# Kernel tuning notes

Measured on AMD Instinct MI355X. Metric: run time of the kernel, lower is better.

Reference implementation:

```python
import jax, jax.numpy as jnp
import numpy as np
from jax import lax

DIM = 1024
DIM_INNER = 2048  # int(dim * expansion_factor)


def log_g(x):
    # log-space g(x): where(x>=0, log(relu(x)+0.5), -softplus(-x))
    return jnp.where(x >= 0, jnp.log(jax.nn.relu(x) + 0.5), -jax.nn.softplus(-x))


def heinsen_associative_scan_log(log_coeffs, log_values):
    # parallel log-space linear recurrence over the sequence axis (axis=1)
    a_star = jnp.cumsum(log_coeffs, axis=1)
    log_h0_plus_b_star = lax.cumlogsumexp(log_values - a_star, axis=1)
    return a_star + log_h0_plus_b_star


def setup_inputs() -> dict:
    key = jax.random.key(0)
    k_x, k_w1, k_w2 = jax.random.split(key, 3)
    x = jax.random.normal(k_x, (4, 4096, DIM), dtype=jnp.float32)
    # Linear(dim, 2*dim_inner, bias=False): store as [in, out] for x @ W
    W_hg = jax.random.normal(k_w1, (DIM, 2 * DIM_INNER), dtype=jnp.float32) * (1.0 / np.sqrt(DIM))
    W_out = jax.random.normal(k_w2, (DIM_INNER, DIM), dtype=jnp.float32) * (1.0 / np.sqrt(DIM_INNER))
    return {"x": x, "W_hg": W_hg, "W_out": W_out}


def reference(x, W_hg, W_out):
    # x: [b, s, dim]
    hg = jnp.einsum('bsd,de->bse', x, W_hg)  # [b, s, 2*dim_inner]
    hidden, gate = jnp.split(hg, 2, axis=-1)
    log_coeffs = -jax.nn.softplus(gate)        # log(1 - z)
    log_z = -jax.nn.softplus(-gate)            # log z
    log_values = log_z + log_g(hidden)
    log_h = heinsen_associative_scan_log(log_coeffs, log_values)  # [b, s, dim_inner]
    out = jnp.exp(log_h)
    return jnp.einsum('bse,ed->bsd', out, W_out)
```

## Files before the change

### kernel.cpp

```cpp
#include <hip/hip_runtime.h>
#include <cmath>

#define DIM 1024
#define DIM_INNER 2048
#define BATCH 4
#define SEQ 4096
#define MTOT (BATCH * SEQ)
#define CHUNK 32
#define NCHUNK (SEQ / CHUNK)

typedef __bf16 bf16x8 __attribute__((ext_vector_type(8)));
typedef short short8_t __attribute__((ext_vector_type(8)));
typedef float floatx4 __attribute__((ext_vector_type(4)));
typedef unsigned short u16x4 __attribute__((ext_vector_type(4)));
typedef unsigned int uint4_t __attribute__((ext_vector_type(4)));
typedef float float4_t __attribute__((ext_vector_type(4)));
typedef unsigned short ushort_t;

template <int N> struct IC { static constexpr int v = N; };
template <bool B> struct BC { static constexpr bool v = B; };

#define LGKM_SB(n) do { asm volatile("s_waitcnt lgkmcnt(" #n ")" ::: "memory"); \
                        __builtin_amdgcn_sched_barrier(0); } while (0)
#define SCHED0() __builtin_amdgcn_sched_barrier(0)
#define SBAR() __builtin_amdgcn_s_barrier()

__device__ __forceinline__ unsigned short f2bf(float f) {
  unsigned int u = __builtin_bit_cast(unsigned int, f);
  u += 0x7fffu + ((u >> 16) & 1u);
  return (unsigned short)(u >> 16);
}
__device__ __forceinline__ float bflo2f(unsigned int u) {
  return __builtin_bit_cast(float, u << 16);
}
__device__ __forceinline__ float bfhi2f(unsigned int u) {
  return __builtin_bit_cast(float, u & 0xffff0000u);
}

__device__ __forceinline__ void lclv_fast(float h, float g, float& lc, float& lv) {
  float eg = __expf(-fabsf(g));
  float sp = fmaxf(g, 0.f) + __logf(1.f + eg);
  lc = -sp;
  float eh = __expf(h);
  float t  = (h >= 0.f) ? (h + 0.5f) : (1.f + eh);
  float lt = __logf(t);
  float lg = (h >= 0.f) ? lt : (h - lt);
  lv = g + lc + lg;
}
__device__ __forceinline__ float logaddexp_f(float a, float b) {
  float m = fmaxf(a, b);
  return m + __logf(1.f + __expf(-fabsf(a - b)));
}

__device__ __forceinline__ void async_copy16(const ushort_t* g, ushort_t* l) {
  __builtin_amdgcn_global_load_lds(
      (const __attribute__((address_space(1))) void*)g,
      (__attribute__((address_space(3))) void*)l, 16, 0, 0);
}

__global__ __launch_bounds__(256) void convert_f32_bf16(
    const float* __restrict__ src, ushort_t* __restrict__ dst) {
  int i = blockIdx.x * 256 + threadIdx.x;
  float4 v = ((const float4*)src)[i];
  u16x4 o = {f2bf(v.x), f2bf(v.y), f2bf(v.z), f2bf(v.w)};
  ((u16x4*)dst)[i] = o;
}

__global__ __launch_bounds__(256) void transpose_f32_bf16(
    const float* __restrict__ src, ushort_t* __restrict__ dst, int K, int N) {
  __shared__ float tile[32][33];
  int tx = threadIdx.x & 31, ty = threadIdx.x >> 5;
  int n0 = blockIdx.x * 32, k0 = blockIdx.y * 32;
#pragma unroll
  for (int i = 0; i < 4; i++) {
    int k = ty + i * 8;
    tile[k][tx] = src[(size_t)(k0 + k) * N + n0 + tx];
  }
  __syncthreads();
#pragma unroll
  for (int i = 0; i < 4; i++) {
    int r = ty + i * 8;
    dst[(size_t)(n0 + r) * K + k0 + tx] = f2bf(tile[tx][r]);
  }
}

#define G1_NT (DIM / 64)
#define G2_NT (DIM_INNER / 64)

__global__ __launch_bounds__(512, 2) void gemm1_fused(
    const ushort_t* __restrict__ Xbf, const ushort_t* __restrict__ Wt,
    unsigned int* __restrict__ LCLV,
    float* __restrict__ Asum, float* __restrict__ Lend, int nbch) {
  __shared__ __align__(16) ushort_t lds[81920];

  const int tid = threadIdx.x;
  const int wv = tid >> 6;
  const int lane = tid & 63;
  const int wr = wv >> 2;
  const int wc = wv & 3;
  const int l15 = lane & 15;
  const int quad = lane >> 4;

  const int nwg = gridDim.x * gridDim.y;
  const int lin = blockIdx.y * gridDim.x + blockIdx.x;
  const int qchunk = nwg >> 3;
  const int wid = (lin & 7) * qchunk + (lin >> 3);
  const int n0 = (wid & 15) * 128;
  const int m0 = (wid >> 4) * 256;

  int aSrc[2][2], bSrc[2][2];
  int dstE[2];
#pragma unroll
  for (int L = 0; L < 2; L++) {
    int e = L * 512 + tid;
    int row = e >> 3, slot = e & 7;
    int sw = (slot ^ (row & 7)) << 3;
    dstE[L] = e * 8;
#pragma unroll
    for (int half = 0; half < 2; half++) {
      aSrc[half][L] = (m0 + half * 128 + row) * DIM + sw;
      int br = half * 128 + row;
      int grow = n0 + ((br >> 6) << 5) + (br & 31) + ((br & 32) ? DIM_INNER : 0);
      bSrc[half][L] = grow * DIM + sw;
    }
  }

  auto stageA = [&](int kt, int half, int buf) {
#pragma unroll
    for (int L = 0; L < 2; L++)
      async_copy16(Xbf + aSrc[half][L] + kt * 64,
                   lds + buf * 16384 + half * 8192 + dstE[L]);
  };
  auto stageB = [&](int kt, int half, int buf) {
#pragma unroll
    for (int L = 0; L < 2; L++)
      async_copy16(Wt + bSrc[half][L] + kt * 64,
                   lds + 49152 + buf * 16384 + half * 8192 + dstE[L]);
  };

  const int swz0 = ((quad ^ (l15 & 7)) << 3);
  const int swz1 = (((4 | quad) ^ (l15 & 7)) << 3);
  const int aB0 = wr * 8192 + l15 * 64 + swz0;
  const int aB1 = wr * 8192 + l15 * 64 + swz1;
  const int bB0 = wc * 4096 + l15 * 64 + swz0;
  const int bB1 = wc * 4096 + l15 * 64 + swz1;

  auto readA = [&](int buf, int mf, int ks) -> bf16x8 {
    const ushort_t* p = lds + buf * 16384 + (ks ? aB1 : aB0) + mf * 1024;
    return __builtin_bit_cast(bf16x8, *(const short8_t*)p);
  };
  auto readB = [&](int buf, int nf, int ks) -> bf16x8 {
    const ushort_t* p = lds + 49152 + buf * 16384 + (ks ? bB1 : bB0) + nf * 1024;
    return __builtin_bit_cast(bf16x8, *(const short8_t*)p);
  };

  floatx4 acc[8][4];
#pragma unroll
  for (int i = 0; i < 8; i++)
#pragma unroll
    for (int j = 0; j < 4; j++) acc[i][j] = (floatx4){0.f, 0.f, 0.f, 0.f};

  bf16x8 aF[4][2], b0F[2][2], b1F[2][2];

  auto mma4 = [&](auto MA, auto MC, auto J, bf16x8 (&bX)[2][2]) {
#pragma unroll
    for (int jj = 0; jj < 2; jj++)
#pragma unroll
      for (int ks = 0; ks < 2; ks++)
        acc[MC.v][J.v + jj] = __builtin_amdgcn_mfma_f32_16x16x32_bf16(
            aF[MA.v][ks], bX[jj][ks], acc[MC.v][J.v + jj], 0, 0, 0);
  };
  auto mmaRow = [&](auto J, bf16x8 (&bvec)[2]) {
#pragma unroll
    for (int m = 0; m < 4; m++)
#pragma unroll
      for (int ks = 0; ks < 2; ks++)
        acc[m][J.v] = __builtin_amdgcn_mfma_f32_16x16x32_bf16(
            aF[m][ks], bvec[ks], acc[m][J.v], 0, 0, 0);
  };

  int bufA = 0, bufB = 0, bufAn = 2, bufBn = 1;

  auto tileBody = [&](int kb, int ka, auto STB, auto STA, auto VMALL) {
    aF[0][0] = readA(bufA, 0, 0); aF[0][1] = readA(bufA, 0, 1);
    b0F[0][0] = readB(bufB, 0, 0); b0F[0][1] = readB(bufB, 0, 1);
    b0F[1][0] = readB(bufB, 1, 0); b0F[1][1] = readB(bufB, 1, 1);
    SCHED0();
    aF[1][0] = readA(bufA, 1, 0); aF[1][1] = readA(bufA, 1, 1);
    SCHED0();
    aF[2][0] = readA(bufA, 2, 0); aF[2][1] = readA(bufA, 2, 1);
    SCHED0();
    aF[3][0] = readA(bufA, 3, 0); aF[3][1] = readA(bufA, 3, 1);
    SCHED0();
    if constexpr (STB.v) stageB(kb, 0, bufBn);
    SBAR();
    __builtin_amdgcn_s_setprio(1);
    LGKM_SB(6); mma4(IC<0>{}, IC<0>{}, IC<0>{}, b0F);
    LGKM_SB(4); mma4(IC<1>{}, IC<1>{}, IC<0>{}, b0F);
    LGKM_SB(2); mma4(IC<2>{}, IC<2>{}, IC<0>{}, b0F);
    LGKM_SB(0); mma4(IC<3>{}, IC<3>{}, IC<0>{}, b0F);
    __builtin_amdgcn_s_setprio(0);
    SBAR();

    b1F[0][0] = readB(bufB, 2, 0); b1F[0][1] = readB(bufB, 2, 1);
    SCHED0();
    b1F[1][0] = readB(bufB, 3, 0); b1F[1][1] = readB(bufB, 3, 1);
    SCHED0();
    if constexpr (STB.v) stageB(kb, 1, bufBn);
    SBAR();
    __builtin_amdgcn_s_setprio(1);
    LGKM_SB(2); mmaRow(IC<2>{}, b1F[0]);
    LGKM_SB(0); mmaRow(IC<3>{}, b1F[1]);
    __builtin_amdgcn_s_setprio(0);
    SBAR();

    aF[0][0] = readA(bufA, 4, 0); aF[0][1] = readA(bufA, 4, 1);
    SCHED0();
    aF[1][0] = readA(bufA, 5, 0); aF[1][1] = readA(bufA, 5, 1);
    SCHED0();
    aF[2][0] = readA(bufA, 6, 0); aF[2][1] = readA(bufA, 6, 1);
    SCHED0();
    aF[3][0] = readA(bufA, 7, 0); aF[3][1] = readA(bufA, 7, 1);
    SCHED0();
    if constexpr (STA.v) stageA(ka, 0, bufAn);
    SBAR();
    __builtin_amdgcn_s_setprio(1);
    LGKM_SB(6); mma4(IC<0>{}, IC<4>{}, IC<2>{}, b1F);
    LGKM_SB(4); mma4(IC<1>{}, IC<5>{}, IC<2>{}, b1F);
    LGKM_SB(2); mma4(IC<2>{}, IC<6>{}, IC<2>{}, b1F);
    LGKM_SB(0); mma4(IC<3>{}, IC<7>{}, IC<2>{}, b1F);
    __builtin_amdgcn_s_setprio(0);
    SBAR();

    if constexpr (STA.v) stageA(ka, 1, bufAn);
    SCHED0();
    if constexpr (STA.v) {
      asm volatile("s_waitcnt vmcnt(4)" ::: "memory");
    } else if constexpr (VMALL.v) {
      asm volatile("s_waitcnt vmcnt(0)" ::: "memory");
    }
    SBAR();
    __builtin_amdgcn_s_setprio(1);
    mma4(IC<0>{}, IC<4>{}, IC<0>{}, b0F);
    mma4(IC<1>{}, IC<5>{}, IC<0>{}, b0F);
    mma4(IC<2>{}, IC<6>{}, IC<0>{}, b0F);
    mma4(IC<3>{}, IC<7>{}, IC<0>{}, b0F);
    __builtin_amdgcn_s_setprio(0);
    SBAR();
  };

  stageB(0, 0, 0); stageB(0, 1, 0);
  stageA(0, 0, 0); stageA(0, 1, 0);
  stageA(1, 0, 1); stageA(1, 1, 1);
  asm volatile("s_waitcnt vmcnt(4)" ::: "memory");
  SBAR();

  for (int u = 0; u < G1_NT - 2; u++) {
    tileBody(u + 1, u + 2, BC<true>{}, BC<true>{}, BC<false>{});
    bufA = (bufA == 2) ? 0 : bufA + 1;
    bufAn = (bufAn == 2) ? 0 : bufAn + 1;
    bufB ^= 1; bufBn ^= 1;
  }
  tileBody(G1_NT - 1, 0, BC<true>{}, BC<false>{}, BC<true>{});
  bufA = (bufA == 2) ? 0 : bufA + 1;
  bufB ^= 1;
  tileBody(0, 0, BC<false>{}, BC<false>{}, BC<false>{});

#pragma unroll
  for (int c2 = 0; c2 < 4; c2++) {
    float hA[2][2], hL[2][2];
#pragma unroll
    for (int mh = 0; mh < 2; mh++) {
      int mf = c2 * 2 + mh;
#pragma unroll
      for (int j = 0; j < 2; j++) {
        int col = n0 + wc * 32 + j * 16 + l15;
        float sA = 0.f, sL = -INFINITY;
#pragma unroll
        for (int r = 0; r < 4; r++) {
          int row = m0 + wr * 128 + mf * 16 + quad * 4 + r;
          float lc, lv;
          lclv_fast(acc[mf][j][r], acc[mf][j + 2][r], lc, lv);
          unsigned int pk = ((unsigned int)f2bf(lv) << 16) | (unsigned int)f2bf(lc);
          LCLV[(size_t)row * DIM_INNER + col] = pk;
          float lcr = bflo2f(pk), lvr = bfhi2f(pk);
          sL = logaddexp_f(sL + lcr, lvr);
          sA += lcr;
        }
        float A = sA, L = sL;
#pragma unroll
        for (int st = 16; st <= 32; st <<= 1) {
          float Ao = __shfl_xor(A, st, 64);
          float Lo = __shfl_xor(L, st, 64);
          bool upper = (lane & st) != 0;
          L = upper ? logaddexp_f(Lo + A, L) : logaddexp_f(L + Ao, Lo);
          A = A + Ao;
        }
        hA[mh][j] = A;
        hL[mh][j] = L;
      }
    }
#pragma unroll
    for (int j = 0; j < 2; j++) {
      float A = hA[0][j] + hA[1][j];
      float L = logaddexp_f(hL[0][j] + hA[1][j], hL[1][j]);
      if (quad == 0) {
        int cg = (m0 + wr * 128 + c2 * 32) >> 5;
        int bz = cg >> 7;
        int cs = cg & (NCHUNK - 1);
        int col = n0 + wc * 32 + j * 16 + l15;
        size_t sidx = (size_t)cs * nbch + (size_t)bz * DIM_INNER + col;
        Asum[sidx] = A;
        Lend[sidx] = L;
      }
    }
  }
}

__global__ __launch_bounds__(512, 2) void gemm2(
    const ushort_t* __restrict__ Hbf, const ushort_t* __restrict__ Wot,
    float* __restrict__ OUT) {
  __shared__ __align__(16) ushort_t lds[81920];

  const int tid = threadIdx.x;
  const int wv = tid >> 6;
  const int lane = tid & 63;
  const int wr = wv >> 2;
  const int wc = wv & 3;
  const int l15 = lane & 15;
  const int quad = lane >> 4;
  const int n0 = blockIdx.x * 256;
  const int m0 = blockIdx.y * 256;

  int aSrc[2][2], bSrc[2][2];
  int dstE[2];
#pragma unroll
  for (int L = 0; L < 2; L++) {
    int e = L * 512 + tid;
    int row = e >> 3, slot = e & 7;
    int sw = (slot ^ (row & 7)) << 3;
    dstE[L] = e * 8;
#pragma unroll
    for (int half = 0; half < 2; half++) {
      aSrc[half][L] = (m0 + half * 128 + row) * DIM_INNER + sw;
      bSrc[half][L] = (n0 + half * 128 + row) * DIM_INNER + sw;
    }
  }

  auto stageA = [&](int kt, int half, int buf) {
#pragma unroll
    for (int L = 0; L < 2; L++)
      async_copy16(Hbf + aSrc[half][L] + kt * 64,
                   lds + buf * 16384 + half * 8192 + dstE[L]);
  };
  auto stageB = [&](int kt, int half, int buf) {
#pragma unroll
    for (int L = 0; L < 2; L++)
      async_copy16(Wot + bSrc[half][L] + kt * 64,
                   lds + 49152 + buf * 16384 + half * 8192 + dstE[L]);
  };

  const int swz0 = ((quad ^ (l15 & 7)) << 3);
  const int swz1 = (((4 | quad) ^ (l15 & 7)) << 3);
  const int aB0 = wr * 8192 + l15 * 64 + swz0;
  const int aB1 = wr * 8192 + l15 * 64 + swz1;
  const int bB0 = wc * 4096 + l15 * 64 + swz0;
  const int bB1 = wc * 4096 + l15 * 64 + swz1;

  auto readA = [&](int buf, int mf, int ks) -> bf16x8 {
    const ushort_t* p = lds + buf * 16384 + (ks ? aB1 : aB0) + mf * 1024;
    return __builtin_bit_cast(bf16x8, *(const short8_t*)p);
  };
  auto readB = [&](int buf, int nf, int ks) -> bf16x8 {
    const ushort_t* p = lds + 49152 + buf * 16384 + (ks ? bB1 : bB0) + nf * 1024;
    return __builtin_bit_cast(bf16x8, *(const short8_t*)p);
  };

  floatx4 acc[8][4];
#pragma unroll
  for (int i = 0; i < 8; i++)
#pragma unroll
    for (int j = 0; j < 4; j++) acc[i][j] = (floatx4){0.f, 0.f, 0.f, 0.f};

  bf16x8 aF[4][2], b0F[2][2], b1F[2][2];

  auto mma4 = [&](auto MA, auto MC, auto J, bf16x8 (&bX)[2][2]) {
#pragma unroll
    for (int jj = 0; jj < 2; jj++)
#pragma unroll
      for (int ks = 0; ks < 2; ks++)
        acc[MC.v][J.v + jj] = __builtin_amdgcn_mfma_f32_16x16x32_bf16(
            aF[MA.v][ks], bX[jj][ks], acc[MC.v][J.v + jj], 0, 0, 0);
  };
  auto mmaRow = [&](auto J, bf16x8 (&bvec)[2]) {
#pragma unroll
    for (int m = 0; m < 4; m++)
#pragma unroll
      for (int ks = 0; ks < 2; ks++)
        acc[m][J.v] = __builtin_amdgcn_mfma_f32_16x16x32_bf16(
            aF[m][ks], bvec[ks], acc[m][J.v], 0, 0, 0);
  };

  int bufA = 0, bufB = 0, bufAn = 2, bufBn = 1;

  auto tileBody = [&](int kb, int ka, auto STB, auto STA, auto VMALL) {
    aF[0][0] = readA(bufA, 0, 0); aF[0][1] = readA(bufA, 0, 1);
    b0F[0][0] = readB(bufB, 0, 0); b0F[0][1] = readB(bufB, 0, 1);
    b0F[1][0] = readB(bufB, 1, 0); b0F[1][1] = readB(bufB, 1, 1);
    SCHED0();
    aF[1][0] = readA(bufA, 1, 0); aF[1][1] = readA(bufA, 1, 1);
    SCHED0();
    aF[2][0] = readA(bufA, 2, 0); aF[2][1] = readA(bufA, 2, 1);
    SCHED0();
    aF[3][0] = readA(bufA, 3, 0); aF[3][1] = readA(bufA, 3, 1);
    SCHED0();
    if constexpr (STB.v) stageB(kb, 0, bufBn);
    SBAR();
    __builtin_amdgcn_s_setprio(1);
    LGKM_SB(6); mma4(IC<0>{}, IC<0>{}, IC<0>{}, b0F);
    LGKM_SB(4); mma4(IC<1>{}, IC<1>{}, IC<0>{}, b0F);
    LGKM_SB(2); mma4(IC<2>{}, IC<2>{}, IC<0>{}, b0F);
    LGKM_SB(0); mma4(IC<3>{}, IC<3>{}, IC<0>{}, b0F);
    __builtin_amdgcn_s_setprio(0);
    SBAR();

    b1F[0][0] = readB(bufB, 2, 0); b1F[0][1] = readB(bufB, 2, 1);
    SCHED0();
    b1F[1][0] = readB(bufB, 3, 0); b1F[1][1] = readB(bufB, 3, 1);
    SCHED0();
    if constexpr (STB.v) stageB(kb, 1, bufBn);
    SBAR();
    __builtin_amdgcn_s_setprio(1);
    LGKM_SB(2); mmaRow(IC<2>{}, b1F[0]);
    LGKM_SB(0); mmaRow(IC<3>{}, b1F[1]);
    __builtin_amdgcn_s_setprio(0);
    SBAR();

    aF[0][0] = readA(bufA, 4, 0); aF[0][1] = readA(bufA, 4, 1);
    SCHED0();
    aF[1][0] = readA(bufA, 5, 0); aF[1][1] = readA(bufA, 5, 1);
    SCHED0();
    aF[2][0] = readA(bufA, 6, 0); aF[2][1] = readA(bufA, 6, 1);
    SCHED0();
    aF[3][0] = readA(bufA, 7, 0); aF[3][1] = readA(bufA, 7, 1);
    SCHED0();
    if constexpr (STA.v) stageA(ka, 0, bufAn);
    SBAR();
    __builtin_amdgcn_s_setprio(1);
    LGKM_SB(6); mma4(IC<0>{}, IC<4>{}, IC<2>{}, b1F);
    LGKM_SB(4); mma4(IC<1>{}, IC<5>{}, IC<2>{}, b1F);
    LGKM_SB(2); mma4(IC<2>{}, IC<6>{}, IC<2>{}, b1F);
    LGKM_SB(0); mma4(IC<3>{}, IC<7>{}, IC<2>{}, b1F);
    __builtin_amdgcn_s_setprio(0);
    SBAR();

    if constexpr (STA.v) stageA(ka, 1, bufAn);
    SCHED0();
    if constexpr (STA.v) {
      asm volatile("s_waitcnt vmcnt(4)" ::: "memory");
    } else if constexpr (VMALL.v) {
      asm volatile("s_waitcnt vmcnt(0)" ::: "memory");
    }
    SBAR();
    __builtin_amdgcn_s_setprio(1);
    mma4(IC<0>{}, IC<4>{}, IC<0>{}, b0F);
    mma4(IC<1>{}, IC<5>{}, IC<0>{}, b0F);
    mma4(IC<2>{}, IC<6>{}, IC<0>{}, b0F);
    mma4(IC<3>{}, IC<7>{}, IC<0>{}, b0F);
    __builtin_amdgcn_s_setprio(0);
    SBAR();
  };

  stageB(0, 0, 0); stageB(0, 1, 0);
  stageA(0, 0, 0); stageA(0, 1, 0);
  stageA(1, 0, 1); stageA(1, 1, 1);
  asm volatile("s_waitcnt vmcnt(4)" ::: "memory");
  SBAR();

  for (int u = 0; u < G2_NT - 2; u++) {
    tileBody(u + 1, u + 2, BC<true>{}, BC<true>{}, BC<false>{});
    bufA = (bufA == 2) ? 0 : bufA + 1;
    bufAn = (bufAn == 2) ? 0 : bufAn + 1;
    bufB ^= 1; bufBn ^= 1;
  }
  tileBody(G2_NT - 1, 0, BC<true>{}, BC<false>{}, BC<true>{});
  bufA = (bufA == 2) ? 0 : bufA + 1;
  bufB ^= 1;
  tileBody(0, 0, BC<false>{}, BC<false>{}, BC<false>{});

#pragma unroll
  for (int mf = 0; mf < 8; mf++)
#pragma unroll
    for (int j = 0; j < 4; j++) {
      int col = n0 + wc * 64 + (j >> 1) * 32 + (j & 1) * 16 + l15;
#pragma unroll
      for (int r = 0; r < 4; r++) {
        int row = m0 + wr * 128 + mf * 16 + quad * 4 + r;
        OUT[(size_t)row * DIM + col] = acc[mf][j][r];
      }
    }
}


__global__ __launch_bounds__(256) void scan_phase2(
    float* Asum, const float* __restrict__ Lend, int nbch) {
  int ch = blockIdx.x * 256 + threadIdx.x;
  float p = -INFINITY;
  for (int c = 0; c < NCHUNK; c++) {
    float a = Asum[(size_t)c * nbch + ch];
    float le = Lend[(size_t)c * nbch + ch];
    Asum[(size_t)c * nbch + ch] = p;
    p = logaddexp_f(a + p, le);
  }
}

__global__ __launch_bounds__(256) void scan_phase3(
    const unsigned int* __restrict__ LCLV, const float* __restrict__ P,
    ushort_t* __restrict__ H, int nbch) {
  const int EQ = DIM_INNER / 4;
  int tid = blockIdx.x * 256 + threadIdx.x;
  int ep = tid % EQ;
  int tmp = tid / EQ;
  int c = tmp % NCHUNK;
  int bz = tmp / NCHUNK;
  size_t base4 = ((size_t)bz * SEQ + (size_t)c * CHUNK) * EQ + ep;
  const uint4_t* L4 = (const uint4_t*)LCLV;
  u16x4* H4 = (u16x4*)H;

  size_t pidx = ((size_t)c * nbch + (size_t)bz * DIM_INNER) / 4 + ep;
  float4_t logh = ((const float4_t*)P)[pidx];
#pragma unroll 4
  for (int t = 0; t < CHUNK; t++) {
    uint4_t u = L4[base4 + (size_t)t * EQ];
    u16x4 hv;
#pragma unroll
    for (int k = 0; k < 4; k++) {
      float lc = bflo2f(u[k]), lv = bfhi2f(u[k]);
      logh[k] = logaddexp_f(lc + logh[k], lv);
      hv[k] = f2bf(__expf(logh[k]));
    }
    H4[base4 + (size_t)t * EQ] = hv;
  }
}

extern "C" void kernel_launch(void* const* d_in, const int* in_sizes, int n_in,
                              void* d_out, int out_size, void* d_ws, size_t ws_size,
                              hipStream_t stream) {
  const float* X = (const float*)d_in[0];
  const float* Whg = (const float*)d_in[1];
  const float* Wout = (const float*)d_in[2];
  float* out = (float*)d_out;

  ushort_t* Xbf = (ushort_t*)d_ws;
  ushort_t* Whg_t = Xbf + (size_t)MTOT * DIM;
  ushort_t* Wout_t = Whg_t + (size_t)(2 * DIM_INNER) * DIM;
  char* pp = (char*)(Wout_t + (size_t)DIM * DIM_INNER);

  const size_t fixed_bytes = (size_t)MTOT * DIM * 2 +
                             (size_t)2 * DIM_INNER * DIM * 2 +
                             (size_t)DIM * DIM_INNER * 2;
  const size_t per_batch = (size_t)SEQ * DIM_INNER * 4 +
                           (size_t)SEQ * DIM_INNER * 2 +
                           2 * (size_t)DIM_INNER * NCHUNK * 4;
  int nb = 4;
  while (nb > 1 && fixed_bytes + (size_t)nb * per_batch > ws_size) nb >>= 1;
  const int npass = BATCH / nb;

  convert_f32_bf16<<<(MTOT * DIM / 4) / 256, 256, 0, stream>>>(X, Xbf);
  transpose_f32_bf16<<<dim3(2 * DIM_INNER / 32, DIM / 32), 256, 0, stream>>>(
      Whg, Whg_t, DIM, 2 * DIM_INNER);
  transpose_f32_bf16<<<dim3(DIM / 32, DIM_INNER / 32), 256, 0, stream>>>(
      Wout, Wout_t, DIM_INNER, DIM);

  for (int pass = 0; pass < npass; pass++) {
    const int b0 = pass * nb;
    const int nrows = nb * SEQ;
    const int nbch = nb * DIM_INNER;

    unsigned int* LCLV = (unsigned int*)pp;
    ushort_t* Hbf = (ushort_t*)(LCLV + (size_t)nb * SEQ * DIM_INNER);
    float* Asum = (float*)(Hbf + (size_t)nb * SEQ * DIM_INNER);
    float* Lend = Asum + (size_t)nb * DIM_INNER * NCHUNK;

    gemm1_fused<<<dim3(DIM_INNER / 128, nrows / 256), 512, 0, stream>>>(
        Xbf + (size_t)b0 * SEQ * DIM, Whg_t, LCLV, Asum, Lend, nbch);
    scan_phase2<<<nbch / 256, 256, 0, stream>>>(Asum, Lend, nbch);
    scan_phase3<<<(nbch / 4 * NCHUNK) / 256, 256, 0, stream>>>(LCLV, Asum, Hbf, nbch);
    gemm2<<<dim3(DIM / 256, nrows / 256), 512, 0, stream>>>(
        Hbf, Wout_t, out + (size_t)b0 * SEQ * DIM);
  }
}
```

Measured before the change: 451.8 us.

## Restructure GEMM pipelines into unrolled double-buffered pairs with fixed LDS offsets

Both GEMM kernels move from a 3-stage A / 2-stage B rotating buffer to a plain double buffer with compile-time LDS offsets. The main loop is unrolled two k-tiles at a time, and each pair does eight quarter MFMA blocks with barrier-separated prefetches. LDS use drops from 160KB to 128KB per block, and the XCD-aware workgroup remapping in gemm1 is removed. The scan carry now uses unrounded fp32 lc/lv instead of the bf16-rounded values, which slightly changes numerics and may also shift cache locality.

```diff
diff --git a/kernel.cpp b/kernel.cpp
--- a/kernel.cpp
+++ b/kernel.cpp
@@ -24,6 +24,8 @@
                         __builtin_amdgcn_sched_barrier(0); } while (0)
 #define SCHED0() __builtin_amdgcn_sched_barrier(0)
 #define SBAR() __builtin_amdgcn_s_barrier()
+#define PRIO1() __builtin_amdgcn_s_setprio(1)
+#define PRIO0() __builtin_amdgcn_s_setprio(0)
 
 __device__ __forceinline__ unsigned short f2bf(float f) {
   unsigned int u = __builtin_bit_cast(unsigned int, f);
@@ -86,27 +88,26 @@
 
 #define G1_NT (DIM / 64)
 #define G2_NT (DIM_INNER / 64)
+#define A0OFF 0
+#define A1OFF 16384
+#define B0OFF 32768
+#define B1OFF 49152
 
 __global__ __launch_bounds__(512, 2) void gemm1_fused(
     const ushort_t* __restrict__ Xbf, const ushort_t* __restrict__ Wt,
     unsigned int* __restrict__ LCLV,
     float* __restrict__ Asum, float* __restrict__ Lend, int nbch) {
-  __shared__ __align__(16) ushort_t lds[81920];
+  __shared__ __align__(16) ushort_t lds[65536];
 
   const int tid = threadIdx.x;
+  const int lane = tid & 63;
   const int wv = tid >> 6;
-  const int lane = tid & 63;
   const int wr = wv >> 2;
   const int wc = wv & 3;
   const int l15 = lane & 15;
   const int quad = lane >> 4;
-
-  const int nwg = gridDim.x * gridDim.y;
-  const int lin = blockIdx.y * gridDim.x + blockIdx.x;
-  const int qchunk = nwg >> 3;
-  const int wid = (lin & 7) * qchunk + (lin >> 3);
-  const int n0 = (wid & 15) * 128;
-  const int m0 = (wid >> 4) * 256;
+  const int n0 = blockIdx.x * 128;
+  const int m0 = blockIdx.y * 256;
 
   int aSrc[2][2], bSrc[2][2];
   int dstE[2];
@@ -125,17 +126,17 @@
     }
   }
 
-  auto stageA = [&](int kt, int half, int buf) {
+  auto stA = [&](int kt, int half, auto AO) {
 #pragma unroll
     for (int L = 0; L < 2; L++)
       async_copy16(Xbf + aSrc[half][L] + kt * 64,
-                   lds + buf * 16384 + half * 8192 + dstE[L]);
-  };
-  auto stageB = [&](int kt, int half, int buf) {
+                   lds + AO.v + half * 8192 + dstE[L]);
+  };
+  auto stB = [&](int kt, int half, auto BO) {
 #pragma unroll
     for (int L = 0; L < 2; L++)
       async_copy16(Wt + bSrc[half][L] + kt * 64,
-                   lds + 49152 + buf * 16384 + half * 8192 + dstE[L]);
+                   lds + BO.v + half * 8192 + dstE[L]);
   };
 
   const int swz0 = ((quad ^ (l15 & 7)) << 3);
@@ -145,15 +146,6 @@
   const int bB0 = wc * 4096 + l15 * 64 + swz0;
   const int bB1 = wc * 4096 + l15 * 64 + swz1;
 
-  auto readA = [&](int buf, int mf, int ks) -> bf16x8 {
-    const ushort_t* p = lds + buf * 16384 + (ks ? aB1 : aB0) + mf * 1024;
-    return __builtin_bit_cast(bf16x8, *(const short8_t*)p);
-  };
-  auto readB = [&](int buf, int nf, int ks) -> bf16x8 {
-    const ushort_t* p = lds + 49152 + buf * 16384 + (ks ? bB1 : bB0) + nf * 1024;
-    return __builtin_bit_cast(bf16x8, *(const short8_t*)p);
-  };
-
   floatx4 acc[8][4];
 #pragma unroll
   for (int i = 0; i < 8; i++)
@@ -162,109 +154,100 @@
 
   bf16x8 aF[4][2], b0F[2][2], b1F[2][2];
 
-  auto mma4 = [&](auto MA, auto MC, auto J, bf16x8 (&bX)[2][2]) {
-#pragma unroll
-    for (int jj = 0; jj < 2; jj++)
-#pragma unroll
-      for (int ks = 0; ks < 2; ks++)
-        acc[MC.v][J.v + jj] = __builtin_amdgcn_mfma_f32_16x16x32_bf16(
-            aF[MA.v][ks], bX[jj][ks], acc[MC.v][J.v + jj], 0, 0, 0);
-  };
-  auto mmaRow = [&](auto J, bf16x8 (&bvec)[2]) {
+  auto rdA4 = [&](auto AO, int mb) {
+#pragma unroll
+    for (int m = 0; m < 4; m++) {
+      aF[m][0] = __builtin_bit_cast(bf16x8,
+          *(const short8_t*)(lds + AO.v + aB0 + (mb + m) * 1024));
+      aF[m][1] = __builtin_bit_cast(bf16x8,
+          *(const short8_t*)(lds + AO.v + aB1 + (mb + m) * 1024));
+    }
+  };
+  auto rdB2 = [&](auto BO, int nb, bf16x8 (&bX)[2][2]) {
+#pragma unroll
+    for (int n = 0; n < 2; n++) {
+      bX[n][0] = __builtin_bit_cast(bf16x8,
+          *(const short8_t*)(lds + BO.v + bB0 + (nb + n) * 1024));
+      bX[n][1] = __builtin_bit_cast(bf16x8,
+          *(const short8_t*)(lds + BO.v + bB1 + (nb + n) * 1024));
+    }
+  };
+  auto mmaQ = [&](auto MB, auto JB, bf16x8 (&bX)[2][2]) {
 #pragma unroll
     for (int m = 0; m < 4; m++)
 #pragma unroll
-      for (int ks = 0; ks < 2; ks++)
-        acc[m][J.v] = __builtin_amdgcn_mfma_f32_16x16x32_bf16(
-            aF[m][ks], bvec[ks], acc[m][J.v], 0, 0, 0);
-  };
-
-  int bufA = 0, bufB = 0, bufAn = 2, bufBn = 1;
-
-  auto tileBody = [&](int kb, int ka, auto STB, auto STA, auto VMALL) {
-    aF[0][0] = readA(bufA, 0, 0); aF[0][1] = readA(bufA, 0, 1);
-    b0F[0][0] = readB(bufB, 0, 0); b0F[0][1] = readB(bufB, 0, 1);
-    b0F[1][0] = readB(bufB, 1, 0); b0F[1][1] = readB(bufB, 1, 1);
-    SCHED0();
-    aF[1][0] = readA(bufA, 1, 0); aF[1][1] = readA(bufA, 1, 1);
-    SCHED0();
-    aF[2][0] = readA(bufA, 2, 0); aF[2][1] = readA(bufA, 2, 1);
-    SCHED0();
-    aF[3][0] = readA(bufA, 3, 0); aF[3][1] = readA(bufA, 3, 1);
-    SCHED0();
-    if constexpr (STB.v) stageB(kb, 0, bufBn);
-    SBAR();
-    __builtin_amdgcn_s_setprio(1);
-    LGKM_SB(6); mma4(IC<0>{}, IC<0>{}, IC<0>{}, b0F);
-    LGKM_SB(4); mma4(IC<1>{}, IC<1>{}, IC<0>{}, b0F);
-    LGKM_SB(2); mma4(IC<2>{}, IC<2>{}, IC<0>{}, b0F);
-    LGKM_SB(0); mma4(IC<3>{}, IC<3>{}, IC<0>{}, b0F);
-    __builtin_amdgcn_s_setprio(0);
-    SBAR();
-
-    b1F[0][0] = readB(bufB, 2, 0); b1F[0][1] = readB(bufB, 2, 1);
-    SCHED0();
-    b1F[1][0] = readB(bufB, 3, 0); b1F[1][1] = readB(bufB, 3, 1);
-    SCHED0();
-    if constexpr (STB.v) stageB(kb, 1, bufBn);
-    SBAR();
-    __builtin_amdgcn_s_setprio(1);
-    LGKM_SB(2); mmaRow(IC<2>{}, b1F[0]);
-    LGKM_SB(0); mmaRow(IC<3>{}, b1F[1]);
-    __builtin_amdgcn_s_setprio(0);
-    SBAR();
-
-    aF[0][0] = readA(bufA, 4, 0); aF[0][1] = readA(bufA, 4, 1);
-    SCHED0();
-    aF[1][0] = readA(bufA, 5, 0); aF[1][1] = readA(bufA, 5, 1);
-    SCHED0();
-    aF[2][0] = readA(bufA, 6, 0); aF[2][1] = readA(bufA, 6, 1);
-    SCHED0();
-    aF[3][0] = readA(bufA, 7, 0); aF[3][1] = readA(bufA, 7, 1);
-    SCHED0();
-    if constexpr (STA.v) stageA(ka, 0, bufAn);
-    SBAR();
-    __builtin_amdgcn_s_setprio(1);
-    LGKM_SB(6); mma4(IC<0>{}, IC<4>{}, IC<2>{}, b1F);
-    LGKM_SB(4); mma4(IC<1>{}, IC<5>{}, IC<2>{}, b1F);
-    LGKM_SB(2); mma4(IC<2>{}, IC<6>{}, IC<2>{}, b1F);
-    LGKM_SB(0); mma4(IC<3>{}, IC<7>{}, IC<2>{}, b1F);
-    __builtin_amdgcn_s_setprio(0);
-    SBAR();
-
-    if constexpr (STA.v) stageA(ka, 1, bufAn);
-    SCHED0();
-    if constexpr (STA.v) {
+      for (int jj = 0; jj < 2; jj++)
+#pragma unroll
+        for (int ks = 0; ks < 2; ks++)
+          acc[MB.v + m][JB.v + jj] = __builtin_amdgcn_mfma_f32_16x16x32_bf16(
+              aF[m][ks], bX[jj][ks], acc[MB.v + m][JB.v + jj], 0, 0, 0);
+  };
+
+  auto pairBody = [&](int k2, auto STG) {
+    rdA4(IC<A0OFF>{}, 0); rdB2(IC<B0OFF>{}, 0, b0F);
+    SCHED0();
+    SBAR(); LGKM_SB(0);
+    PRIO1(); mmaQ(IC<0>{}, IC<0>{}, b0F); PRIO0();
+    SBAR();
+    rdB2(IC<B0OFF>{}, 2, b1F);
+    SCHED0();
+    SBAR(); LGKM_SB(0);
+    PRIO1(); mmaQ(IC<0>{}, IC<2>{}, b1F); PRIO0();
+    SBAR();
+    rdA4(IC<A0OFF>{}, 4);
+    SCHED0();
+    if constexpr (STG.v) stB(k2, 0, IC<B0OFF>{});
+    SBAR(); LGKM_SB(0);
+    PRIO1(); mmaQ(IC<4>{}, IC<2>{}, b1F); PRIO0();
+    SBAR();
+    if constexpr (STG.v) {
+      stB(k2, 1, IC<B0OFF>{});
       asm volatile("s_waitcnt vmcnt(4)" ::: "memory");
-    } else if constexpr (VMALL.v) {
+    } else {
       asm volatile("s_waitcnt vmcnt(0)" ::: "memory");
     }
     SBAR();
-    __builtin_amdgcn_s_setprio(1);
-    mma4(IC<0>{}, IC<4>{}, IC<0>{}, b0F);
-    mma4(IC<1>{}, IC<5>{}, IC<0>{}, b0F);
-    mma4(IC<2>{}, IC<6>{}, IC<0>{}, b0F);
-    mma4(IC<3>{}, IC<7>{}, IC<0>{}, b0F);
-    __builtin_amdgcn_s_setprio(0);
-    SBAR();
-  };
-
-  stageB(0, 0, 0); stageB(0, 1, 0);
-  stageA(0, 0, 0); stageA(0, 1, 0);
-  stageA(1, 0, 1); stageA(1, 1, 1);
-  asm volatile("s_waitcnt vmcnt(4)" ::: "memory");
+    PRIO1(); mmaQ(IC<4>{}, IC<0>{}, b0F); PRIO0();
+    SBAR();
+    rdA4(IC<A1OFF>{}, 0); rdB2(IC<B1OFF>{}, 0, b0F);
+    SCHED0();
+    if constexpr (STG.v) stA(k2, 0, IC<A0OFF>{});
+    SBAR(); LGKM_SB(0);
+    PRIO1(); mmaQ(IC<0>{}, IC<0>{}, b0F); PRIO0();
+    SBAR();
+    rdB2(IC<B1OFF>{}, 2, b1F);
+    SCHED0();
+    if constexpr (STG.v) stA(k2, 1, IC<A0OFF>{});
+    SBAR(); LGKM_SB(0);
+    PRIO1(); mmaQ(IC<0>{}, IC<2>{}, b1F); PRIO0();
+    SBAR();
+    rdA4(IC<A1OFF>{}, 4);
+    SCHED0();
+    if constexpr (STG.v) stB(k2 + 1, 0, IC<B1OFF>{});
+    SBAR(); LGKM_SB(0);
+    PRIO1(); mmaQ(IC<4>{}, IC<2>{}, b1F); PRIO0();
+    SBAR();
+    if constexpr (STG.v) {
+      stB(k2 + 1, 1, IC<B1OFF>{});
+      stA(k2 + 1, 0, IC<A1OFF>{});
+      stA(k2 + 1, 1, IC<A1OFF>{});
+      asm volatile("s_waitcnt vmcnt(8)" ::: "memory");
+    }
+    SBAR();
+    PRIO1(); mmaQ(IC<4>{}, IC<0>{}, b0F); PRIO0();
+    SBAR();
+  };
+
+  stA(0, 0, IC<A0OFF>{}); stA(0, 1, IC<A0OFF>{});
+  stB(0, 0, IC<B0OFF>{}); stB(0, 1, IC<B0OFF>{});
+  stA(1, 0, IC<A1OFF>{}); stA(1, 1, IC<A1OFF>{});
+  stB(1, 0, IC<B1OFF>{}); stB(1, 1, IC<B1OFF>{});
+  asm volatile("s_waitcnt vmcnt(8)" ::: "memory");
   SBAR();
 
-  for (int u = 0; u < G1_NT - 2; u++) {
-    tileBody(u + 1, u + 2, BC<true>{}, BC<true>{}, BC<false>{});
-    bufA = (bufA == 2) ? 0 : bufA + 1;
-    bufAn = (bufAn == 2) ? 0 : bufAn + 1;
-    bufB ^= 1; bufBn ^= 1;
-  }
-  tileBody(G1_NT - 1, 0, BC<true>{}, BC<false>{}, BC<true>{});
-  bufA = (bufA == 2) ? 0 : bufA + 1;
-  bufB ^= 1;
-  tileBody(0, 0, BC<false>{}, BC<false>{}, BC<false>{});
+  for (int it = 0; it < G1_NT / 2 - 1; ++it)
+    pairBody(2 * it + 2, BC<true>{});
+  pairBody(0, BC<false>{});
 
 #pragma unroll
   for (int c2 = 0; c2 < 4; c2++) {
@@ -283,9 +266,8 @@
           lclv_fast(acc[mf][j][r], acc[mf][j + 2][r], lc, lv);
           unsigned int pk = ((unsigned int)f2bf(lv) << 16) | (unsigned int)f2bf(lc);
           LCLV[(size_t)row * DIM_INNER + col] = pk;
-          float lcr = bflo2f(pk), lvr = bfhi2f(pk);
-          sL = logaddexp_f(sL + lcr, lvr);
-          sA += lcr;
+          sL = logaddexp_f(sL + lc, lv);
+          sA += lc;
         }
         float A = sA, L = sL;
 #pragma unroll
@@ -320,11 +302,11 @@
 __global__ __launch_bounds__(512, 2) void gemm2(
     const ushort_t* __restrict__ Hbf, const ushort_t* __restrict__ Wot,
     float* __restrict__ OUT) {
-  __shared__ __align__(16) ushort_t lds[81920];
+  __shared__ __align__(16) ushort_t lds[65536];
 
   const int tid = threadIdx.x;
+  const int lane = tid & 63;
   const int wv = tid >> 6;
-  const int lane = tid & 63;
   const int wr = wv >> 2;
   const int wc = wv & 3;
   const int l15 = lane & 15;
@@ -347,17 +329,17 @@
     }
   }
 
-  auto stageA = [&](int kt, int half, int buf) {
+  auto stA = [&](int kt, int half, auto AO) {
 #pragma unroll
     for (int L = 0; L < 2; L++)
       async_copy16(Hbf + aSrc[half][L] + kt * 64,
-                   lds + buf * 16384 + half * 8192 + dstE[L]);
-  };
-  auto stageB = [&](int kt, int half, int buf) {
+                   lds + AO.v + half * 8192 + dstE[L]);
+  };
+  auto stB = [&](int kt, int half, auto BO) {
 #pragma unroll
     for (int L = 0; L < 2; L++)
       async_copy16(Wot + bSrc[half][L] + kt * 64,
-                   lds + 49152 + buf * 16384 + half * 8192 + dstE[L]);
+                   lds + BO.v + half * 8192 + dstE[L]);
   };
 
   const int swz0 = ((quad ^ (l15 & 7)) << 3);
@@ -367,15 +349,6 @@
   const int bB0 = wc * 4096 + l15 * 64 + swz0;
   const int bB1 = wc * 4096 + l15 * 64 + swz1;
 
-  auto readA = [&](int buf, int mf, int ks) -> bf16x8 {
-    const ushort_t* p = lds + buf * 16384 + (ks ? aB1 : aB0) + mf * 1024;
-    return __builtin_bit_cast(bf16x8, *(const short8_t*)p);
-  };
-  auto readB = [&](int buf, int nf, int ks) -> bf16x8 {
-    const ushort_t* p = lds + 49152 + buf * 16384 + (ks ? bB1 : bB0) + nf * 1024;
-    return __builtin_bit_cast(bf16x8, *(const short8_t*)p);
-  };
-
   floatx4 acc[8][4];
 #pragma unroll
   for (int i = 0; i < 8; i++)
@@ -384,109 +357,100 @@
 
   bf16x8 aF[4][2], b0F[2][2], b1F[2][2];
 
-  auto mma4 = [&](auto MA, auto MC, auto J, bf16x8 (&bX)[2][2]) {
-#pragma unroll
-    for (int jj = 0; jj < 2; jj++)
-#pragma unroll
-      for (int ks = 0; ks < 2; ks++)
-        acc[MC.v][J.v + jj] = __builtin_amdgcn_mfma_f32_16x16x32_bf16(
-            aF[MA.v][ks], bX[jj][ks], acc[MC.v][J.v + jj], 0, 0, 0);
-  };
-  auto mmaRow = [&](auto J, bf16x8 (&bvec)[2]) {
+  auto rdA4 = [&](auto AO, int mb) {
+#pragma unroll
+    for (int m = 0; m < 4; m++) {
+      aF[m][0] = __builtin_bit_cast(bf16x8,
+          *(const short8_t*)(lds + AO.v + aB0 + (mb + m) * 1024));
+      aF[m][1] = __builtin_bit_cast(bf16x8,
+          *(const short8_t*)(lds + AO.v + aB1 + (mb + m) * 1024));
+    }
+  };
+  auto rdB2 = [&](auto BO, int nb, bf16x8 (&bX)[2][2]) {
+#pragma unroll
+    for (int n = 0; n < 2; n++) {
+      bX[n][0] = __builtin_bit_cast(bf16x8,
+          *(const short8_t*)(lds + BO.v + bB0 + (nb + n) * 1024));
+      bX[n][1] = __builtin_bit_cast(bf16x8,
+          *(const short8_t*)(lds + BO.v + bB1 + (nb + n) * 1024));
+    }
+  };
+  auto mmaQ = [&](auto MB, auto JB, bf16x8 (&bX)[2][2]) {
 #pragma unroll
     for (int m = 0; m < 4; m++)
 #pragma unroll
-      for (int ks = 0; ks < 2; ks++)
-        acc[m][J.v] = __builtin_amdgcn_mfma_f32_16x16x32_bf16(
-            aF[m][ks], bvec[ks], acc[m][J.v], 0, 0, 0);
-  };
-
-  int bufA = 0, bufB = 0, bufAn = 2, bufBn = 1;
-
-  auto tileBody = [&](int kb, int ka, auto STB, auto STA, auto VMALL) {
-    aF[0][0] = readA(bufA, 0, 0); aF[0][1] = readA(bufA, 0, 1);
-    b0F[0][0] = readB(bufB, 0, 0); b0F[0][1] = readB(bufB, 0, 1);
-    b0F[1][0] = readB(bufB, 1, 0); b0F[1][1] = readB(bufB, 1, 1);
-    SCHED0();
-    aF[1][0] = readA(bufA, 1, 0); aF[1][1] = readA(bufA, 1, 1);
-    SCHED0();
-    aF[2][0] = readA(bufA, 2, 0); aF[2][1] = readA(bufA, 2, 1);
-    SCHED0();
-    aF[3][0] = readA(bufA, 3, 0); aF[3][1] = readA(bufA, 3, 1);
-    SCHED0();
-    if constexpr (STB.v) stageB(kb, 0, bufBn);
-    SBAR();
-    __builtin_amdgcn_s_setprio(1);
-    LGKM_SB(6); mma4(IC<0>{}, IC<0>{}, IC<0>{}, b0F);
-    LGKM_SB(4); mma4(IC<1>{}, IC<1>{}, IC<0>{}, b0F);
-    LGKM_SB(2); mma4(IC<2>{}, IC<2>{}, IC<0>{}, b0F);
-    LGKM_SB(0); mma4(IC<3>{}, IC<3>{}, IC<0>{}, b0F);
-    __builtin_amdgcn_s_setprio(0);
-    SBAR();
-
-    b1F[0][0] = readB(bufB, 2, 0); b1F[0][1] = readB(bufB, 2, 1);
-    SCHED0();
-    b1F[1][0] = readB(bufB, 3, 0); b1F[1][1] = readB(bufB, 3, 1);
-    SCHED0();
-    if constexpr (STB.v) stageB(kb, 1, bufBn);
-    SBAR();
-    __builtin_amdgcn_s_setprio(1);
-    LGKM_SB(2); mmaRow(IC<2>{}, b1F[0]);
-    LGKM_SB(0); mmaRow(IC<3>{}, b1F[1]);
-    __builtin_amdgcn_s_setprio(0);
-    SBAR();
-
-    aF[0][0] = readA(bufA, 4, 0); aF[0][1] = readA(bufA, 4, 1);
-    SCHED0();
-    aF[1][0] = readA(bufA, 5, 0); aF[1][1] = readA(bufA, 5, 1);
-    SCHED0();
-    aF[2][0] = readA(bufA, 6, 0); aF[2][1] = readA(bufA, 6, 1);
-    SCHED0();
-    aF[3][0] = readA(bufA, 7, 0); aF[3][1] = readA(bufA, 7, 1);
-    SCHED0();
-    if constexpr (STA.v) stageA(ka, 0, bufAn);
-    SBAR();
-    __builtin_amdgcn_s_setprio(1);
-    LGKM_SB(6); mma4(IC<0>{}, IC<4>{}, IC<2>{}, b1F);
-    LGKM_SB(4); mma4(IC<1>{}, IC<5>{}, IC<2>{}, b1F);
-    LGKM_SB(2); mma4(IC<2>{}, IC<6>{}, IC<2>{}, b1F);
-    LGKM_SB(0); mma4(IC<3>{}, IC<7>{}, IC<2>{}, b1F);
-    __builtin_amdgcn_s_setprio(0);
-    SBAR();
-
-    if constexpr (STA.v) stageA(ka, 1, bufAn);
-    SCHED0();
-    if constexpr (STA.v) {
+      for (int jj = 0; jj < 2; jj++)
+#pragma unroll
+        for (int ks = 0; ks < 2; ks++)
+          acc[MB.v + m][JB.v + jj] = __builtin_amdgcn_mfma_f32_16x16x32_bf16(
+              aF[m][ks], bX[jj][ks], acc[MB.v + m][JB.v + jj], 0, 0, 0);
+  };
+
+  auto pairBody = [&](int k2, auto STG) {
+    rdA4(IC<A0OFF>{}, 0); rdB2(IC<B0OFF>{}, 0, b0F);
+    SCHED0();
+    SBAR(); LGKM_SB(0);
+    PRIO1(); mmaQ(IC<0>{}, IC<0>{}, b0F); PRIO0();
+    SBAR();
+    rdB2(IC<B0OFF>{}, 2, b1F);
+    SCHED0();
+    SBAR(); LGKM_SB(0);
+    PRIO1(); mmaQ(IC<0>{}, IC<2>{}, b1F); PRIO0();
+    SBAR();
+    rdA4(IC<A0OFF>{}, 4);
+    SCHED0();
+    if constexpr (STG.v) stB(k2, 0, IC<B0OFF>{});
+    SBAR(); LGKM_SB(0);
+    PRIO1(); mmaQ(IC<4>{}, IC<2>{}, b1F); PRIO0();
+    SBAR();
+    if constexpr (STG.v) {
+      stB(k2, 1, IC<B0OFF>{});
       asm volatile("s_waitcnt vmcnt(4)" ::: "memory");
-    } else if constexpr (VMALL.v) {
+    } else {
       asm volatile("s_waitcnt vmcnt(0)" ::: "memory");
     }
     SBAR();
-    __builtin_amdgcn_s_setprio(1);
-    mma4(IC<0>{}, IC<4>{}, IC<0>{}, b0F);
-    mma4(IC<1>{}, IC<5>{}, IC<0>{}, b0F);
-    mma4(IC<2>{}, IC<6>{}, IC<0>{}, b0F);
-    mma4(IC<3>{}, IC<7>{}, IC<0>{}, b0F);
-    __builtin_amdgcn_s_setprio(0);
-    SBAR();
-  };
-
-  stageB(0, 0, 0); stageB(0, 1, 0);
-  stageA(0, 0, 0); stageA(0, 1, 0);
-  stageA(1, 0, 1); stageA(1, 1, 1);
-  asm volatile("s_waitcnt vmcnt(4)" ::: "memory");
+    PRIO1(); mmaQ(IC<4>{}, IC<0>{}, b0F); PRIO0();
+    SBAR();
+    rdA4(IC<A1OFF>{}, 0); rdB2(IC<B1OFF>{}, 0, b0F);
+    SCHED0();
+    if constexpr (STG.v) stA(k2, 0, IC<A0OFF>{});
+    SBAR(); LGKM_SB(0);
+    PRIO1(); mmaQ(IC<0>{}, IC<0>{}, b0F); PRIO0();
+    SBAR();
+    rdB2(IC<B1OFF>{}, 2, b1F);
+    SCHED0();
+    if constexpr (STG.v) stA(k2, 1, IC<A0OFF>{});
+    SBAR(); LGKM_SB(0);
+    PRIO1(); mmaQ(IC<0>{}, IC<2>{}, b1F); PRIO0();
+    SBAR();
+    rdA4(IC<A1OFF>{}, 4);
+    SCHED0();
+    if constexpr (STG.v) stB(k2 + 1, 0, IC<B1OFF>{});
+    SBAR(); LGKM_SB(0);
+    PRIO1(); mmaQ(IC<4>{}, IC<2>{}, b1F); PRIO0();
+    SBAR();
+    if constexpr (STG.v) {
+      stB(k2 + 1, 1, IC<B1OFF>{});
+      stA(k2 + 1, 0, IC<A1OFF>{});
+      stA(k2 + 1, 1, IC<A1OFF>{});
+      asm volatile("s_waitcnt vmcnt(8)" ::: "memory");
+    }
+    SBAR();
+    PRIO1(); mmaQ(IC<4>{}, IC<0>{}, b0F); PRIO0();
+    SBAR();
+  };
+
+  stA(0, 0, IC<A0OFF>{}); stA(0, 1, IC<A0OFF>{});
+  stB(0, 0, IC<B0OFF>{}); stB(0, 1, IC<B0OFF>{});
+  stA(1, 0, IC<A1OFF>{}); stA(1, 1, IC<A1OFF>{});
+  stB(1, 0, IC<B1OFF>{}); stB(1, 1, IC<B1OFF>{});
+  asm volatile("s_waitcnt vmcnt(8)" ::: "memory");
   SBAR();
 
-  for (int u = 0; u < G2_NT - 2; u++) {
-    tileBody(u + 1, u + 2, BC<true>{}, BC<true>{}, BC<false>{});
-    bufA = (bufA == 2) ? 0 : bufA + 1;
-    bufAn = (bufAn == 2) ? 0 : bufAn + 1;
-    bufB ^= 1; bufBn ^= 1;
-  }
-  tileBody(G2_NT - 1, 0, BC<true>{}, BC<false>{}, BC<true>{});
-  bufA = (bufA == 2) ? 0 : bufA + 1;
-  bufB ^= 1;
-  tileBody(0, 0, BC<false>{}, BC<false>{}, BC<false>{});
+  for (int it = 0; it < G2_NT / 2 - 1; ++it)
+    pairBody(2 * it + 2, BC<true>{});
+  pairBody(0, BC<false>{});
 
 #pragma unroll
   for (int mf = 0; mf < 8; mf++)
```

New measurement: 451.5 us. About the same (-0.1%).
